# Kernel optimization log

Hardware: AMD Instinct MI355X
Metric: run time of the kernel (lower is better)

The kernel has to match this reference:

```python
import jax, jax.numpy as jnp
import numpy as np

GRID = 112  # densepose predictor output resolution (hardcoded in forward)
D = 16      # CSE embedding dim (view(16, -1) in forward)


def setup_inputs() -> dict:
    key = jax.random.key(0)
    k1, k2 = jax.random.split(key)
    feats = jax.random.normal(k1, (2, D, GRID, GRID), dtype=jnp.float32)
    vertex_embeddings = jax.random.normal(k2, (27554, D), dtype=jnp.float32)
    return {"feats": feats, "vertex_embeddings": vertex_embeddings}


def reference(feats, vertex_embeddings):
    # feats: [B, 16, 112, 112]; vertex_embeddings: [M, 16]
    B = feats.shape[0]
    # per-pixel embeddings: [B, N, D] with N = 112*112 (matches feats[i].view(16,-1).T)
    x = feats.reshape(B, D, -1).transpose(0, 2, 1)
    x2 = jnp.sum(x * x, axis=-1, keepdims=True)            # [B, N, 1]
    v2 = jnp.sum(vertex_embeddings * vertex_embeddings, -1)  # [M]
    dist = x2 - 2.0 * jnp.einsum('bnd,md->bnm', x, vertex_embeddings) + v2
    dps = jnp.argmin(dist, axis=-1).reshape(B, GRID, GRID)  # [B, 112, 112] int
    return feats, dps
```

## Files before the change

kernel.cpp:

```cpp
#include <hip/hip_runtime.h>
#include <math.h>
#include <float.h>

#define GRIDP 112
#define NPIX (GRIDP * GRIDP)
#define D 16
#define TSA 3328
#define TSB 3072
#define G 2
#define TG 2
#define GRPB (TG * TSA)
#define GRPB_PAD 7168
#define NISS 7

typedef short s16x8 __attribute__((ext_vector_type(8)));
typedef float f32x16 __attribute__((ext_vector_type(16)));
typedef unsigned int uint32;
typedef unsigned long long u64;
typedef const __attribute__((address_space(1))) uint32* gas_ptr;
typedef __attribute__((address_space(3))) uint32* las_ptr;

__device__ inline unsigned short f2bf(float x) {
    unsigned u = __float_as_uint(x);
    u += 0x7fffu + ((u >> 16) & 1u);
    return (unsigned short)(u >> 16);
}
__device__ inline float bf2f(unsigned short b) { return __uint_as_float(((unsigned)b) << 16); }

#define MFMA __builtin_amdgcn_mfma_f32_32x32x16_bf16

__device__ inline unsigned fmap(float f) {
    unsigned b = __float_as_uint(f);
    return (b & 0x80000000u) ? ~b : (b | 0x80000000u);
}

__device__ __forceinline__ void split_store_row(const float* x, char* base, int row) {
    unsigned short t0[D], t1[D], t2[D];
#pragma unroll
    for (int e = 0; e < D; ++e) {
        float v = x[e];
        unsigned short a = f2bf(v);  float r1 = v - bf2f(a);
        unsigned short b = f2bf(r1); float r2 = r1 - bf2f(b);
        t0[e] = a; t1[e] = b; t2[e] = f2bf(r2);
    }
#pragma unroll
    for (int h2 = 0; h2 < 2; ++h2) {
        char* p = base + h2 * 512 + row * 16;
        s16x8 v0, v1, v2s;
#pragma unroll
        for (int j = 0; j < 8; ++j) {
            v0[j] = (short)t0[h2 * 8 + j];
            v1[j] = (short)t1[h2 * 8 + j];
            v2s[j] = (short)t2[h2 * 8 + j];
        }
        *(s16x8*)(p)        = v0;
        *(s16x8*)(p + 1024) = v1;
        *(s16x8*)(p + 2048) = v2s;
    }
}

__global__ __launch_bounds__(256) void prep_fused(
    const float* __restrict__ verts, const float* __restrict__ feats,
    char* __restrict__ abuf, char* __restrict__ bbuf,
    float* __restrict__ v2p, float* __restrict__ outf, u64* __restrict__ keys,
    int M, int Mtiles, int NP, int PTiles, int nvb, int npb, int ncb, int nf4)
{
    int bx = blockIdx.x;
    if (bx < nvb) {
        int mp = bx * 256 + threadIdx.x;
        if (mp >= Mtiles * 32) return;
        int tile = mp >> 5, row = mp & 31;
        float x[D]; float v2;
        if (mp < M) {
            const float4* r4 = (const float4*)(verts + (size_t)mp * D);
            float4 a = r4[0], b = r4[1], c = r4[2], d = r4[3];
            x[0]=a.x; x[1]=a.y; x[2]=a.z; x[3]=a.w;
            x[4]=b.x; x[5]=b.y; x[6]=b.z; x[7]=b.w;
            x[8]=c.x; x[9]=c.y; x[10]=c.z; x[11]=c.w;
            x[12]=d.x; x[13]=d.y; x[14]=d.z; x[15]=d.w;
            float s = 0.f;
#pragma unroll
            for (int e = 0; e < D; ++e) s = fmaf(x[e], x[e], s);
            v2 = s;
            v2p[mp] = s;
        } else {
#pragma unroll
            for (int e = 0; e < D; ++e) x[e] = 0.f;
            v2 = FLT_MAX;
        }
        size_t tb = (size_t)tile * TSA;
        int hv = (row >> 2) & 1, rv = (row & 3) + 4 * (row >> 3);
        *(float*)(abuf + tb + 3072 + hv * 64 + rv * 4) = v2;
        split_store_row(x, abuf + tb, row);
    } else if (bx < nvb + npb) {
        int p = (bx - nvb) * 256 + threadIdx.x;
        if (p >= PTiles * 32) return;
        int tile = p >> 5, colr = p & 31;
        float x[D];
        if (p < NP) {
            int b = p / NPIX, n = p - b * NPIX;
            const float* xf = feats + ((size_t)b * D) * NPIX + n;
#pragma unroll
            for (int e = 0; e < D; ++e) x[e] = -2.0f * xf[(size_t)e * NPIX];
        } else {
#pragma unroll
            for (int e = 0; e < D; ++e) x[e] = 0.f;
        }
        split_store_row(x, bbuf + (size_t)tile * TSB, colr);
    } else if (bx < nvb + npb + ncb) {
        int i = (bx - nvb - npb) * 256 + threadIdx.x;
        if (i < nf4)
            ((float4*)outf)[i] = ((const float4*)feats)[i];
    } else {
        int i = (bx - nvb - npb - ncb) * 256 + threadIdx.x;
        if (i < NP) keys[i] = ~0ull;
    }
}

__device__ inline float mintree16(const f32x16& a) {
    float a0 = fminf(fminf(a[0],  a[1]),  a[2]);
    float a1 = fminf(fminf(a[3],  a[4]),  a[5]);
    float a2 = fminf(fminf(a[6],  a[7]),  a[8]);
    float a3 = fminf(fminf(a[9],  a[10]), a[11]);
    float a4 = fminf(fminf(a[12], a[13]), a[14]);
    float a5 = fminf(fminf(a0, a1), a[15]);
    float a6 = fminf(fminf(a2, a3), a4);
    return fminf(a5, a6);
}

__device__ __forceinline__ void stage_group(const char* gbase, char* lbase,
                                            int wid, int lane) {
    for (int i = wid; i < NISS; i += 4) {
        __builtin_amdgcn_global_load_lds(
            (gas_ptr)(gbase + i * 1024 + lane * 16),
            (las_ptr)(lbase + i * 1024),
            16, 0, 0);
    }
}

struct AFrag { s16x8 ah, am, al; f32x16 c; };

__device__ __forceinline__ AFrag load_frag(const char* lt, int h, int col) {
    AFrag f;
    f.ah = *(const s16x8*)(lt + (size_t)h * 512 + (size_t)col * 16);
    f.am = *(const s16x8*)(lt + 1024 + (size_t)h * 512 + (size_t)col * 16);
    f.al = *(const s16x8*)(lt + 2048 + (size_t)h * 512 + (size_t)col * 16);
    f.c  = *(const f32x16*)(lt + 3072 + (size_t)h * 64);
    return f;
}

__device__ __forceinline__ void chain_mfma(
    const AFrag& f, const s16x8* bh, const s16x8* bm, const s16x8* bl,
    f32x16* acc)
{
#pragma unroll
    for (int g = 0; g < G; ++g) acc[g] = MFMA(f.ah, bh[g], f.c, 0, 0, 0);
#pragma unroll
    for (int g = 0; g < G; ++g) acc[g] = MFMA(f.ah, bm[g], acc[g], 0, 0, 0);
#pragma unroll
    for (int g = 0; g < G; ++g) acc[g] = MFMA(f.am, bh[g], acc[g], 0, 0, 0);
#pragma unroll
    for (int g = 0; g < G; ++g) acc[g] = MFMA(f.ah, bl[g], acc[g], 0, 0, 0);
#pragma unroll
    for (int g = 0; g < G; ++g) acc[g] = MFMA(f.am, bm[g], acc[g], 0, 0, 0);
#pragma unroll
    for (int g = 0; g < G; ++g) acc[g] = MFMA(f.al, bh[g], acc[g], 0, 0, 0);
}

__device__ __forceinline__ void tree_upd(
    const f32x16* acc, int mt, float* best, int* btl)
{
#pragma unroll
    for (int g = 0; g < G; ++g) {
        float m = mintree16(acc[g]);
        if (m < best[g]) { btl[g] = mt; best[g] = m; }
    }
}

__global__ __launch_bounds__(256) void mfma_scan(
    const char* __restrict__ abuf, const char* __restrict__ bbuf,
    u64* __restrict__ keys, int Mtiles, int chunk, int NP, int PTiles)
{
    __shared__ __align__(16) char smem[2][GRPB_PAD];
    int lane = threadIdx.x & 63;
    int wid  = threadIdx.x >> 6;
    int col  = lane & 31, h = lane >> 5;
    int ptb  = (blockIdx.x * 4 + wid) * G;

    s16x8 bh[G], bm[G], bl[G];
#pragma unroll
    for (int g = 0; g < G; ++g) {
        int pt = ptb + g;
        int ptc = pt < PTiles ? pt : PTiles - 1;
        const char* bb = bbuf + (size_t)ptc * TSB + (size_t)h * 512 + (size_t)col * 16;
        bh[g] = *(const s16x8*)bb;
        bm[g] = *(const s16x8*)(bb + 1024);
        bl[g] = *(const s16x8*)(bb + 2048);
    }

    int mt0 = blockIdx.y * chunk;
    int mt1 = mt0 + chunk; if (mt1 > Mtiles) mt1 = Mtiles;
    int nT   = mt1 - mt0;
    int nGrp = (nT + TG - 1) / TG;

    float best[G]; int btl[G];
#pragma unroll
    for (int g = 0; g < G; ++g) { best[g] = FLT_MAX; btl[g] = mt0; }

    const char* gsrc = abuf + (size_t)mt0 * TSA;

    stage_group(gsrc, smem[0], wid, lane);
    __syncthreads();

    int cur = 0;
    for (int grp = 0; grp < nGrp; ++grp) {
        if (grp + 1 < nGrp)
            stage_group(gsrc + (size_t)(grp + 1) * GRPB, smem[cur ^ 1], wid, lane);

        const char* lb = smem[cur];
        int mtb = mt0 + grp * TG;
        int rem = nT - grp * TG;
        if (rem >= 2) {
            AFrag f0 = load_frag(lb, h, col);
            AFrag f1 = load_frag(lb + TSA, h, col);
            f32x16 a0[G], a1[G];
            chain_mfma(f0, bh, bm, bl, a0);
            chain_mfma(f1, bh, bm, bl, a1);
            tree_upd(a0, mtb,     best, btl);
            tree_upd(a1, mtb + 1, best, btl);
        } else {
            AFrag f0 = load_frag(lb, h, col);
            f32x16 a0[G];
            chain_mfma(f0, bh, bm, bl, a0);
            tree_upd(a0, mtb, best, btl);
        }
        __syncthreads();
        cur ^= 1;
    }

#pragma unroll
    for (int g = 0; g < G; ++g) {
        float o = __shfl_xor(best[g], 32, 64);
        int  ot = __shfl_xor(btl[g], 32, 64);
        if (o < best[g] || (o == best[g] && ot < btl[g])) { best[g] = o; btl[g] = ot; }
    }
    if (lane < 32) {
#pragma unroll
        for (int g = 0; g < G; ++g) {
            int pt = ptb + g;
            int px = pt * 32 + col;
            if (pt < PTiles && px < NP) {
                u64 key = ((u64)fmap(best[g]) << 32) | (unsigned)btl[g];
                atomicMin(&keys[px], key);
            }
        }
    }
}

__global__ __launch_bounds__(256) void finalize(
    const u64* __restrict__ keys,
    const float* __restrict__ feats, const float* __restrict__ verts,
    const float* __restrict__ v2p, float* __restrict__ dps,
    int NP, int M)
{
    int p = blockIdx.x * 256 + threadIdx.x;
    if (p >= NP) return;
    int bt = (int)(unsigned)(keys[p] & 0xffffffffu);
    int b = p / NPIX, n = p - b * NPIX;
    const float* xf = feats + ((size_t)b * D) * NPIX + n;
    float xs[D];
#pragma unroll
    for (int d2 = 0; d2 < D; ++d2) xs[d2] = -2.0f * xf[(size_t)d2 * NPIX];
    int m0 = bt * 32, m1 = m0 + 32; if (m1 > M) m1 = M;
    float best = FLT_MAX; int bi = m0;
    for (int m = m0; m < m1; ++m) {
        const float4* vr = (const float4*)(verts + (size_t)m * D);
        float4 a = vr[0], bq = vr[1], c = vr[2], d = vr[3];
        float acc = v2p[m];
        acc = fmaf(a.x, xs[0], acc);  acc = fmaf(a.y, xs[1], acc);
        acc = fmaf(a.z, xs[2], acc);  acc = fmaf(a.w, xs[3], acc);
        acc = fmaf(bq.x, xs[4], acc); acc = fmaf(bq.y, xs[5], acc);
        acc = fmaf(bq.z, xs[6], acc); acc = fmaf(bq.w, xs[7], acc);
        acc = fmaf(c.x, xs[8], acc);  acc = fmaf(c.y, xs[9], acc);
        acc = fmaf(c.z, xs[10], acc); acc = fmaf(c.w, xs[11], acc);
        acc = fmaf(d.x, xs[12], acc); acc = fmaf(d.y, xs[13], acc);
        acc = fmaf(d.z, xs[14], acc); acc = fmaf(d.w, xs[15], acc);
        if (acc < best) { best = acc; bi = m; }
    }
    dps[p] = (float)bi;
}

__global__ __launch_bounds__(256) void v2_kernel(const float* __restrict__ verts,
                                                 float* __restrict__ v2, int M) {
    int m = blockIdx.x * 256 + threadIdx.x;
    if (m >= M) return;
    const float4* r = (const float4*)(verts + (size_t)m * D);
    float4 a = r[0], b = r[1], c = r[2], d = r[3];
    v2[m] = ((a.x*a.x + a.y*a.y) + (a.z*a.z + a.w*a.w))
          + ((b.x*b.x + b.y*b.y) + (b.z*b.z + b.w*b.w))
          + ((c.x*c.x + c.y*c.y) + (c.z*c.z + c.w*c.w))
          + ((d.x*d.x + d.y*d.y) + (d.z*d.z + d.w*d.w));
}

__global__ __launch_bounds__(256) void argmin_partial(
    const float* __restrict__ feats, const float* __restrict__ verts,
    const float* __restrict__ v2, float* __restrict__ pval, int* __restrict__ pidx,
    int M, int NPtot, int chunk)
{
    int p = blockIdx.x * 256 + threadIdx.x;
    if (p >= NPtot) return;
    int b = p / NPIX, n = p - b * NPIX;
    const float* xf = feats + ((size_t)b * D) * NPIX + n;
    float x[D];
#pragma unroll
    for (int d2 = 0; d2 < D; ++d2) x[d2] = -2.0f * xf[(size_t)d2 * NPIX];
    int s = blockIdx.y;
    int m0 = s * chunk, m1 = m0 + chunk; if (m1 > M) m1 = M;
    float best = INFINITY; int bi = 0;
    for (int m = m0; m < m1; ++m) {
        const float* vr = verts + (size_t)m * D;
        float acc = v2[m];
#pragma unroll
        for (int d2 = 0; d2 < D; ++d2) acc = fmaf(vr[d2], x[d2], acc);
        if (acc < best) { best = acc; bi = m; }
    }
    pval[(size_t)s * NPtot + p] = best;
    pidx[(size_t)s * NPtot + p] = bi;
}

__global__ __launch_bounds__(256) void reduce_idx(
    const float* __restrict__ pval, const int* __restrict__ pidx,
    float* __restrict__ dps, int S, int NP)
{
    int p = blockIdx.x * 256 + threadIdx.x;
    if (p >= NP) return;
    float bv = pval[p]; int bi = pidx[p];
    for (int s = 1; s < S; ++s) {
        float v = pval[(size_t)s * NP + p];
        int   i = pidx[(size_t)s * NP + p];
        if (v < bv || (v == bv && i < bi)) { bv = v; bi = i; }
    }
    dps[p] = (float)bi;
}

extern "C" void kernel_launch(void* const* d_in, const int* in_sizes, int n_in,
                              void* d_out, int out_size, void* d_ws, size_t ws_size,
                              hipStream_t stream)
{
    const float* feats = (const float*)d_in[0];
    const float* verts = (const float*)d_in[1];
    int M          = in_sizes[1] / D;
    int feat_elems = in_sizes[0];
    int Bn         = feat_elems / (D * NPIX);
    int NP         = Bn * NPIX;
    float* out = (float*)d_out;

    int PTiles = (NP + 31) >> 5;
    int Mtiles = (M + 31) >> 5;

    size_t off = 0;
    auto alloc = [&](size_t sz) { size_t o = off; off = (off + sz + 255) & ~(size_t)255; return o; };
    size_t oBF = alloc((size_t)PTiles * TSB);
    size_t oAF = alloc((size_t)(Mtiles + 4 * TG + 2) * TSA);
    size_t oV2 = alloc((size_t)M * 4);
    size_t oKY = alloc((size_t)NP * 8);
    size_t need = off;

    int S = 32;

    if (need <= ws_size) {
        char*  bbuf = (char*)d_ws + oBF;
        char*  abuf = (char*)d_ws + oAF;
        float* v2p  = (float*)((char*)d_ws + oV2);
        u64*   keys = (u64*)((char*)d_ws + oKY);

        int nvb = (Mtiles * 32 + 255) / 256;
        int npb = (PTiles * 32 + 255) / 256;
        int nf4 = feat_elems / 4;
        int ncb = (nf4 + 255) / 256;
        int nkb = (NP + 255) / 256;
        prep_fused<<<dim3(nvb + npb + ncb + nkb), dim3(256), 0, stream>>>(
            verts, feats, abuf, bbuf, v2p, out, keys,
            M, Mtiles, NP, PTiles, nvb, npb, ncb, nf4);

        int chunk = (Mtiles + S - 1) / S;
        mfma_scan<<<dim3((PTiles + 4 * G - 1) / (4 * G), S), dim3(256), 0, stream>>>(
            abuf, bbuf, keys, Mtiles, chunk, NP, PTiles);

        finalize<<<dim3((NP + 255) / 256), dim3(256), 0, stream>>>(
            keys, feats, verts, v2p, out + feat_elems, NP, M);
    } else {
        hipMemcpyAsync(out, feats, (size_t)feat_elems * sizeof(float),
                       hipMemcpyDeviceToDevice, stream);
        char* ws = (char*)d_ws;
        float* v2 = (float*)ws;
        size_t o2 = (((size_t)M * 4) + 255) & ~(size_t)255;
        int S2 = 16;
        while (S2 > 1 && o2 + (size_t)S2 * NP * 8 > ws_size) S2 >>= 1;
        float* pval = (float*)(ws + o2);
        int*   pidx = (int*)(ws + o2 + (size_t)S2 * NP * 4);
        int chunk = (M + S2 - 1) / S2;
        v2_kernel<<<dim3((M + 255) / 256), dim3(256), 0, stream>>>(verts, v2, M);
        argmin_partial<<<dim3((NP + 255) / 256, S2), dim3(256), 0, stream>>>(
            feats, verts, v2, pval, pidx, M, NP, chunk);
        reduce_idx<<<dim3((NP + 255) / 256), dim3(256), 0, stream>>>(
            pval, pidx, out + feat_elems, S2, NP);
    }
}
```

Baseline: 142.7 us.

## Stage whole per-block vertex chunk into LDS once and double M-split

Replaces the double-buffered per-group streaming of vertex tiles with a single up-front bulk copy of the block's entire chunk (up to 14 tiles, about 46 KB) into LDS, followed by a barrier-free compute loop. The M dimension split is doubled from 32 to 64 blocks so each chunk fits in LDS. This removes the per-iteration __syncthreads and staging overhead, at the cost of a serialized load phase before compute, lower occupancy from the larger LDS footprint, and twice as many atomicMin merges per pixel.

Result: no change. 140.3 us (-1.6%).

```diff
diff --git a/kernel.cpp b/kernel.cpp
--- a/kernel.cpp
+++ b/kernel.cpp
@@ -8,10 +8,9 @@
 #define TSA 3328
 #define TSB 3072
 #define G 2
-#define TG 2
-#define GRPB (TG * TSA)
-#define GRPB_PAD 7168
-#define NISS 7
+#define CHUNK 14
+#define LDSB 47104
+#define NISS 46
 
 typedef short s16x8 __attribute__((ext_vector_type(8)));
 typedef float f32x16 __attribute__((ext_vector_type(16)));
@@ -128,16 +127,6 @@
     return fminf(a5, a6);
 }
 
-__device__ __forceinline__ void stage_group(const char* gbase, char* lbase,
-                                            int wid, int lane) {
-    for (int i = wid; i < NISS; i += 4) {
-        __builtin_amdgcn_global_load_lds(
-            (gas_ptr)(gbase + i * 1024 + lane * 16),
-            (las_ptr)(lbase + i * 1024),
-            16, 0, 0);
-    }
-}
-
 struct AFrag { s16x8 ah, am, al; f32x16 c; };
 
 __device__ __forceinline__ AFrag load_frag(const char* lt, int h, int col) {
@@ -181,7 +170,7 @@
     const char* __restrict__ abuf, const char* __restrict__ bbuf,
     u64* __restrict__ keys, int Mtiles, int chunk, int NP, int PTiles)
 {
-    __shared__ __align__(16) char smem[2][GRPB_PAD];
+    __shared__ __align__(16) char smem[LDSB];
     int lane = threadIdx.x & 63;
     int wid  = threadIdx.x >> 6;
     int col  = lane & 31, h = lane >> 5;
@@ -200,43 +189,39 @@
 
     int mt0 = blockIdx.y * chunk;
     int mt1 = mt0 + chunk; if (mt1 > Mtiles) mt1 = Mtiles;
-    int nT   = mt1 - mt0;
-    int nGrp = (nT + TG - 1) / TG;
+    int nT  = mt1 - mt0;
+
+    const char* gsrc = abuf + (size_t)mt0 * TSA;
+    for (int i = wid; i < NISS; i += 4) {
+        __builtin_amdgcn_global_load_lds(
+            (gas_ptr)(gsrc + i * 1024 + lane * 16),
+            (las_ptr)(smem + i * 1024),
+            16, 0, 0);
+    }
+    __syncthreads();
 
     float best[G]; int btl[G];
 #pragma unroll
     for (int g = 0; g < G; ++g) { best[g] = FLT_MAX; btl[g] = mt0; }
 
-    const char* gsrc = abuf + (size_t)mt0 * TSA;
-
-    stage_group(gsrc, smem[0], wid, lane);
-    __syncthreads();
-
-    int cur = 0;
-    for (int grp = 0; grp < nGrp; ++grp) {
-        if (grp + 1 < nGrp)
-            stage_group(gsrc + (size_t)(grp + 1) * GRPB, smem[cur ^ 1], wid, lane);
-
-        const char* lb = smem[cur];
-        int mtb = mt0 + grp * TG;
-        int rem = nT - grp * TG;
-        if (rem >= 2) {
-            AFrag f0 = load_frag(lb, h, col);
-            AFrag f1 = load_frag(lb + TSA, h, col);
-            f32x16 a0[G], a1[G];
-            chain_mfma(f0, bh, bm, bl, a0);
-            chain_mfma(f1, bh, bm, bl, a1);
-            tree_upd(a0, mtb,     best, btl);
-            tree_upd(a1, mtb + 1, best, btl);
-        } else {
-            AFrag f0 = load_frag(lb, h, col);
-            f32x16 a0[G];
-            chain_mfma(f0, bh, bm, bl, a0);
-            tree_upd(a0, mtb, best, btl);
-        }
-        __syncthreads();
-        cur ^= 1;
-    }
+    int t = 0;
+    for (; t + 1 < nT; t += 2) {
+        AFrag f0 = load_frag(smem + (size_t)t * TSA,       h, col);
+        AFrag f1 = load_frag(smem + (size_t)(t + 1) * TSA, h, col);
+        f32x16 a0[G], a1[G];
+        chain_mfma(f0, bh, bm, bl, a0);
+        chain_mfma(f1, bh, bm, bl, a1);
+        tree_upd(a0, mt0 + t,     best, btl);
+        tree_upd(a1, mt0 + t + 1, best, btl);
+    }
+    if (t < nT) {
+        AFrag f0 = load_frag(smem + (size_t)t * TSA, h, col);
+        f32x16 a0[G];
+        chain_mfma(f0, bh, bm, bl, a0);
+        tree_upd(a0, mt0 + t, best, btl);
+    }
+
+    if (nT <= 0) return;
 
 #pragma unroll
     for (int g = 0; g < G; ++g) {
@@ -358,17 +343,19 @@
     int PTiles = (NP + 31) >> 5;
     int Mtiles = (M + 31) >> 5;
 
+    int S = 64;
+    int chunk = (Mtiles + S - 1) / S;
+    int atiles = S * chunk + 16;
+
     size_t off = 0;
     auto alloc = [&](size_t sz) { size_t o = off; off = (off + sz + 255) & ~(size_t)255; return o; };
     size_t oBF = alloc((size_t)PTiles * TSB);
-    size_t oAF = alloc((size_t)(Mtiles + 4 * TG + 2) * TSA);
+    size_t oAF = alloc((size_t)atiles * TSA);
     size_t oV2 = alloc((size_t)M * 4);
     size_t oKY = alloc((size_t)NP * 8);
     size_t need = off;
 
-    int S = 32;
-
-    if (need <= ws_size) {
+    if (need <= ws_size && chunk <= CHUNK) {
         char*  bbuf = (char*)d_ws + oBF;
         char*  abuf = (char*)d_ws + oAF;
         float* v2p  = (float*)((char*)d_ws + oV2);
@@ -383,7 +370,6 @@
             verts, feats, abuf, bbuf, v2p, out, keys,
             M, Mtiles, NP, PTiles, nvb, npb, ncb, nf4);
 
-        int chunk = (Mtiles + S - 1) / S;
         mfma_scan<<<dim3((PTiles + 4 * G - 1) / (4 * G), S), dim3(256), 0, stream>>>(
             abuf, bbuf, keys, Mtiles, chunk, NP, PTiles);
 
@@ -399,10 +385,10 @@
         while (S2 > 1 && o2 + (size_t)S2 * NP * 8 > ws_size) S2 >>= 1;
         float* pval = (float*)(ws + o2);
         int*   pidx = (int*)(ws + o2 + (size_t)S2 * NP * 4);
-        int chunk = (M + S2 - 1) / S2;
+        int chunk2 = (M + S2 - 1) / S2;
         v2_kernel<<<dim3((M + 255) / 256), dim3(256), 0, stream>>>(verts, v2, M);
         argmin_partial<<<dim3((NP + 255) / 256, S2), dim3(256), 0, stream>>>(
-            feats, verts, v2, pval, pidx, M, NP, chunk);
+            feats, verts, v2, pval, pidx, M, NP, chunk2);
         reduce_idx<<<dim3((NP + 255) / 256), dim3(256), 0, stream>>>(
             pval, pidx, out + feat_elems, S2, NP);
     }
```
